# Optimization experiments

Hardware: AMD Instinct MI355X
Metric: run time of the kernel (lower is better)

## Reference

```python
import jax, jax.numpy as jnp
import numpy as np

H, D, DK, DV = 8, 512, 64, 64
B, L = 2, 2048
LN_EPS = 1e-5


def setup_inputs() -> dict:
    key = jax.random.key(0)
    ks = jax.random.split(key, 12)
    q = jax.random.normal(ks[0], (B, L, D), jnp.float32)
    k = jax.random.normal(ks[1], (B, L, D), jnp.float32)
    v = jax.random.normal(ks[2], (B, L, D), jnp.float32)
    mask = jax.random.randint(ks[3], (H * B, L, L), 0, 2) > 0
    sq = np.sqrt(2.0 / (D + DK)).astype(np.float32)
    sv = np.sqrt(2.0 / (D + DV)).astype(np.float32)
    Wq = jax.random.normal(ks[4], (H * DK, D), jnp.float32) * sq
    Wk = jax.random.normal(ks[5], (H * DK, D), jnp.float32) * sq
    Wv = jax.random.normal(ks[6], (H * DV, D), jnp.float32) * sv
    xav = np.sqrt(2.0 / (H * DV + D)).astype(np.float32)
    Wfc = jax.random.normal(ks[7], (D, H * DV), jnp.float32) * xav
    bfc = jnp.zeros((D,), jnp.float32)
    gamma = jnp.ones((D,), jnp.float32)
    beta = jnp.zeros((D,), jnp.float32)
    return {"q": q, "k": k, "v": v, "mask": mask, "Wq": Wq, "Wk": Wk,
            "Wv": Wv, "Wfc": Wfc, "bfc": bfc, "gamma": gamma, "beta": beta}


def reference(q, k, v, mask, Wq, Wk, Wv, Wfc, bfc, gamma, beta):
    # dropout in eval mode (identity)
    temperature = jnp.sqrt(jnp.asarray(DK, q.dtype))
    residual = q
    # projections -> (H, B, L, dk/dv), matching permute(2,0,1,3)
    qh = (q @ Wq.T).reshape(B, L, H, DK).transpose(2, 0, 1, 3)
    kh = (k @ Wk.T).reshape(B, L, H, DK).transpose(2, 0, 1, 3)
    vh = (v @ Wv.T).reshape(B, L, H, DV).transpose(2, 0, 1, 3)
    attn = jnp.einsum('hbqd,hbkd->hbqk', qh, kh) / temperature
    m = mask.reshape(H, B, L, L)
    attn = jnp.where(m, jnp.asarray(-1e10, attn.dtype), attn)
    attn = jax.nn.softmax(attn, axis=-1)
    out = jnp.einsum('hbqk,hbkd->hbqd', attn, vh)  # (H,B,L,DV)
    out = out.transpose(1, 2, 0, 3).reshape(B, L, H * DV)
    out = out @ Wfc.T + bfc
    x = out + residual
    mu = jnp.mean(x, axis=-1, keepdims=True)
    var = jnp.var(x, axis=-1, keepdims=True)
    return gamma * (x - mu) * jax.lax.rsqrt(var + LN_EPS) + beta
```

## Files before the change

### kernel.cpp

```cpp
#include <hip/hip_runtime.h>
#include <hip/hip_bf16.h>
#include <cmath>
#include <cstdint>

#define H_ 8
#define B_ 2
#define L_ 2048
#define D_ 512
#define SPLIT_ 4

typedef __attribute__((ext_vector_type(8))) short short8_t;
typedef __attribute__((ext_vector_type(4))) float float4_t;
typedef __attribute__((ext_vector_type(4))) unsigned short ushort4_t;
typedef __attribute__((ext_vector_type(2))) unsigned int uint2_t;
typedef __attribute__((ext_vector_type(4))) unsigned int uint4_t;

__device__ __forceinline__ unsigned short bf16u(float f) {
  union { __hip_bfloat16 b; unsigned short u; } c;
  c.b = __float2bfloat16(f);
  return c.u;
}
__device__ __forceinline__ unsigned bf16x2(float lo, float hi) {
  return (unsigned)bf16u(lo) | ((unsigned)bf16u(hi) << 16);
}
__device__ __forceinline__ float bf2f(unsigned short u) {
  union { unsigned u; float f; } c; c.u = (unsigned)u << 16; return c.f;
}

__device__ __forceinline__ unsigned pack8(unsigned long long x) {
  x |= x >> 4; x |= x >> 2; x |= x >> 1;
  x &= 0x0101010101010101ULL;
  return (unsigned)((x * 0x0102040810204080ULL) >> 56);
}

__global__ __launch_bounds__(256)
void cvt_w(const float* __restrict__ wfc, unsigned short* __restrict__ wfcb) {
  int i = (blockIdx.x * 256 + threadIdx.x) * 4;
  float4_t a = *(const float4_t*)(wfc + i);
  ushort4_t o;
  o[0] = bf16u(a[0]); o[1] = bf16u(a[1]); o[2] = bf16u(a[2]); o[3] = bf16u(a[3]);
  *(ushort4_t*)(wfcb + i) = o;
}

__global__ __launch_bounds__(512)
void proj_gemm(const float* __restrict__ q, const float* __restrict__ k,
               const float* __restrict__ v,
               const float* __restrict__ wq, const float* __restrict__ wk,
               const float* __restrict__ wv,
               unsigned short* __restrict__ Qp, unsigned short* __restrict__ Kp,
               unsigned short* __restrict__ Vt) {
  __shared__ unsigned short As[128][72];
  __shared__ unsigned short Bs[64][72];
  const int tid = threadIdx.x, lane = tid & 63, wave = tid >> 6;
  const int g = lane >> 4, qi = lane & 15;
  const int m0 = blockIdx.x * 128, n0 = blockIdx.y * 64;
  const int z = blockIdx.z;
  const float* A = (z == 0) ? q : (z == 1) ? k : v;
  const float* W = (z == 0) ? wq : (z == 1) ? wk : wv;

  float4_t acc[4] = {};
  const int ar = tid >> 2, ac = (tid & 3) * 16;
  const int br = tid >> 3, bc = (tid & 7) * 8;

  for (int kt = 0; kt < 512; kt += 64) {
    const float* src = A + (size_t)(m0 + ar) * 512 + kt + ac;
    float4_t f0 = *(const float4_t*)(src);
    float4_t f1 = *(const float4_t*)(src + 4);
    float4_t f2 = *(const float4_t*)(src + 8);
    float4_t f3 = *(const float4_t*)(src + 12);
    short8_t s0, s1;
    s0[0] = bf16u(f0[0]); s0[1] = bf16u(f0[1]); s0[2] = bf16u(f0[2]); s0[3] = bf16u(f0[3]);
    s0[4] = bf16u(f1[0]); s0[5] = bf16u(f1[1]); s0[6] = bf16u(f1[2]); s0[7] = bf16u(f1[3]);
    s1[0] = bf16u(f2[0]); s1[1] = bf16u(f2[1]); s1[2] = bf16u(f2[2]); s1[3] = bf16u(f2[3]);
    s1[4] = bf16u(f3[0]); s1[5] = bf16u(f3[1]); s1[6] = bf16u(f3[2]); s1[7] = bf16u(f3[3]);
    *(short8_t*)(&As[ar][ac]) = s0;
    *(short8_t*)(&As[ar][ac + 8]) = s1;
    const float* wsrc = W + (size_t)(n0 + br) * 512 + kt + bc;
    float4_t w0 = *(const float4_t*)(wsrc);
    float4_t w1 = *(const float4_t*)(wsrc + 4);
    short8_t sw;
    sw[0] = bf16u(w0[0]); sw[1] = bf16u(w0[1]); sw[2] = bf16u(w0[2]); sw[3] = bf16u(w0[3]);
    sw[4] = bf16u(w1[0]); sw[5] = bf16u(w1[1]); sw[6] = bf16u(w1[2]); sw[7] = bf16u(w1[3]);
    *(short8_t*)(&Bs[br][bc]) = sw;
    __syncthreads();
#pragma unroll
    for (int kk = 0; kk < 2; kk++) {
      const int krow = kk * 32 + g * 8;
      short8_t a = *(const short8_t*)(&As[wave * 16 + qi][krow]);
#pragma unroll
      for (int n = 0; n < 4; n++) {
        short8_t b = *(const short8_t*)(&Bs[n * 16 + qi][krow]);
        acc[n] = __builtin_amdgcn_mfma_f32_16x16x32_bf16(a, b, acc[n], 0, 0, 0);
      }
    }
    __syncthreads();
  }

  const int gmb = m0 + wave * 16 + g * 4;
#pragma unroll
  for (int n = 0; n < 4; n++) {
    int gn = n0 + n * 16 + qi;
    int h = gn >> 6, d = gn & 63;
    if (z == 2) {
      int bb = gmb >> 11, l = gmb & 2047;
      ushort4_t o;
#pragma unroll
      for (int r = 0; r < 4; r++) o[r] = bf16u(acc[n][r]);
      *(ushort4_t*)(Vt + ((size_t)(h * B_ + bb) * 64 + d) * L_ + l) = o;
    } else {
      float sc = (z == 0) ? 0.125f : 1.0f;
      unsigned short* O = (z == 0) ? Qp : Kp;
#pragma unroll
      for (int r = 0; r < 4; r++) {
        int gm = gmb + r;
        int bb = gm >> 11, l = gm & 2047;
        O[((size_t)(h * B_ + bb) * L_ + l) * 64 + d] = bf16u(acc[n][r] * sc);
      }
    }
  }
}

template<int MS>
__device__ __forceinline__ void attn_body(
    const unsigned short* __restrict__ Qp, const unsigned short* __restrict__ Kp,
    const unsigned short* __restrict__ Vt, const unsigned char* __restrict__ mask,
    unsigned short* __restrict__ Opart, float* __restrict__ MLpart,
    unsigned short (*Ks)[72], unsigned short (*Vs)[72], unsigned int (*Ps)[36]) {
  const int tid = threadIdx.x, lane = tid & 63, wave = tid >> 6;
  const int g = lane >> 4, qi = lane & 15;
  const int hb = blockIdx.y;
  const int sp = blockIdx.z;
  const int k_begin = sp * (L_ / SPLIT_), k_end = k_begin + L_ / SPLIT_;
  const int qg0 = blockIdx.x * 128 + wave * 16;
  const int qg = qg0 + qi;
  const size_t base = (size_t)hb * (L_ * 64);

  const size_t mrowoff = ((size_t)hb * L_ + qg0 + (lane >> 2)) * L_;
  const unsigned char* mb1 = mask + mrowoff + (lane & 3) * 16;
  const unsigned* mb4 = (const unsigned*)mask + mrowoff + (lane & 3) * 16;

  short8_t qf[2];
#pragma unroll
  for (int kk = 0; kk < 2; kk++)
    qf[kk] = *(const short8_t*)(Qp + base + (size_t)qg * 64 + kk * 32 + g * 8);

  float4_t o[4] = {};
  float mrun = -INFINITY, lrun = 0.f;
  const int sr = tid >> 3, sc = (tid & 7) * 8;
  const int srcA = qi * 4;

#define LOADFB(dst, kpos)                                                        \
  do {                                                                           \
    if (MS == 1) {                                                               \
      uint4_t x = *(const uint4_t*)(mb1 + (kpos));                               \
      unsigned long long lo = ((unsigned long long)x[1] << 32) | x[0];           \
      unsigned long long hi = ((unsigned long long)x[3] << 32) | x[2];           \
      dst = pack8(lo) | (pack8(hi) << 8);                                        \
    } else {                                                                     \
      dst = 0;                                                                   \
      _Pragma("unroll")                                                          \
      for (int j = 0; j < 4; j++) {                                              \
        uint4_t x = *(const uint4_t*)(mb4 + (kpos) + j * 4);                     \
        dst |= (((unsigned)(x[0] != 0)) | ((unsigned)(x[1] != 0) << 1) |         \
                ((unsigned)(x[2] != 0) << 2) | ((unsigned)(x[3] != 0) << 3))     \
               << (j * 4);                                                       \
      }                                                                          \
    }                                                                            \
  } while (0)

  short8_t kr, vr;
  unsigned fb1, fb2;
  kr = *(const short8_t*)(Kp + base + (size_t)(k_begin + sr) * 64 + sc);
  vr = *(const short8_t*)(Vt + base + (size_t)sr * L_ + k_begin + sc);
  LOADFB(fb1, k_begin);
  fb2 = 0;
  if (k_begin + 64 < k_end) LOADFB(fb2, k_begin + 64);

  for (int k0 = k_begin; k0 < k_end; k0 += 64) {
    *(short8_t*)(&Ks[sr][sc]) = kr;
    *(short8_t*)(&Vs[sr][sc]) = vr;
    unsigned fb_cur = fb1;
    fb1 = fb2;
    __syncthreads();

    if (k0 + 64 < k_end) {
      const int kn = k0 + 64;
      kr = *(const short8_t*)(Kp + base + (size_t)(kn + sr) * 64 + sc);
      vr = *(const short8_t*)(Vt + base + (size_t)sr * L_ + kn + sc);
    }
    if (k0 + 128 < k_end) LOADFB(fb2, k0 + 128);

    unsigned nib[4];
#pragma unroll
    for (int t = 0; t < 4; t++)
      nib[t] = ((unsigned)__shfl((int)fb_cur, srcA + t, 64) >> (g * 4)) & 0xFu;

    float4_t st[4] = {};
#pragma unroll
    for (int kk = 0; kk < 2; kk++) {
      const int krow = kk * 32 + g * 8;
#pragma unroll
      for (int t = 0; t < 4; t++) {
        short8_t a = *(const short8_t*)(&Ks[t * 16 + qi][krow]);
        st[t] = __builtin_amdgcn_mfma_f32_16x16x32_bf16(a, qf[kk], st[t], 0, 0, 0);
      }
    }

    float tmax = -INFINITY;
#pragma unroll
    for (int t = 0; t < 4; t++)
#pragma unroll
      for (int r = 0; r < 4; r++) {
        if ((nib[t] >> r) & 1u) st[t][r] = -1e10f;
        tmax = fmaxf(tmax, st[t][r]);
      }
    tmax = fmaxf(tmax, __shfl_xor(tmax, 16, 64));
    tmax = fmaxf(tmax, __shfl_xor(tmax, 32, 64));

    float nm = fmaxf(mrun, tmax);
    float fac = __expf(mrun - nm);
    mrun = nm;

    float psum = 0.f;
    unsigned w8[4][2];
#pragma unroll
    for (int t = 0; t < 4; t++) {
      float p0 = __expf(st[t][0] - nm);
      float p1 = __expf(st[t][1] - nm);
      float p2 = __expf(st[t][2] - nm);
      float p3 = __expf(st[t][3] - nm);
      psum += (p0 + p1) + (p2 + p3);
      w8[t][0] = bf16x2(p0, p1);
      w8[t][1] = bf16x2(p2, p3);
    }
    psum += __shfl_xor(psum, 16, 64);
    psum += __shfl_xor(psum, 32, 64);
    lrun = lrun * fac + psum;
#pragma unroll
    for (int n2 = 0; n2 < 4; n2++)
#pragma unroll
      for (int r = 0; r < 4; r++) o[n2][r] *= fac;

#pragma unroll
    for (int t = 0; t < 4; t++) {
      uint2_t w2; w2[0] = w8[t][0]; w2[1] = w8[t][1];
      *(uint2_t*)(&Ps[qi][t * 8 + g * 2]) = w2;
    }
#pragma unroll
    for (int s = 0; s < 2; s++) {
      short8_t pb = *(const short8_t*)(&Ps[qi][s * 16 + g * 4]);
#pragma unroll
      for (int n2 = 0; n2 < 4; n2++) {
        short8_t a = *(const short8_t*)(&Vs[n2 * 16 + qi][s * 32 + g * 8]);
        o[n2] = __builtin_amdgcn_mfma_f32_16x16x32_bf16(a, pb, o[n2], 0, 0, 0);
      }
    }
    __syncthreads();
  }
#undef LOADFB

  const size_t pb = (((size_t)sp * 16 + hb) * L_ + qg) * 64;
#pragma unroll
  for (int n2 = 0; n2 < 4; n2++) {
    ushort4_t ov;
#pragma unroll
    for (int r = 0; r < 4; r++) ov[r] = bf16u(o[n2][r]);
    *(ushort4_t*)(Opart + pb + n2 * 16 + g * 4) = ov;
  }
  if (lane < 16) {
    float* ml = MLpart + (((size_t)sp * 16 + hb) * L_ + qg) * 2;
    ml[0] = mrun; ml[1] = lrun;
  }
}

__global__ __launch_bounds__(512)
void attn_split(const unsigned short* __restrict__ Qp, const unsigned short* __restrict__ Kp,
                const unsigned short* __restrict__ Vt, const unsigned char* __restrict__ mask,
                unsigned short* __restrict__ Opart, float* __restrict__ MLpart) {
  __shared__ unsigned short Ks[64][72];
  __shared__ unsigned short Vs[64][72];
  __shared__ unsigned int PsAll[8][16][36];
  const int wave = threadIdx.x >> 6;
  unsigned probe = ((const unsigned*)mask)[threadIdx.x & 63];
  if (__any(probe > 1u))
    attn_body<1>(Qp, Kp, Vt, mask, Opart, MLpart, Ks, Vs, PsAll[wave]);
  else
    attn_body<4>(Qp, Kp, Vt, mask, Opart, MLpart, Ks, Vs, PsAll[wave]);
}

__global__ __launch_bounds__(256)
void attn_combine(const unsigned short* __restrict__ Opart, const float* __restrict__ MLpart,
                  unsigned short* __restrict__ Y) {
  int gid = blockIdx.x * 256 + threadIdx.x;
  int dvc = (gid & 7) * 8;
  int hbq = gid >> 3;
  int hb = hbq >> 11, qq = hbq & 2047;
  int h = hb >> 1, bb = hb & 1;
  float m[SPLIT_], l[SPLIT_];
  float M = -INFINITY;
#pragma unroll
  for (int s = 0; s < SPLIT_; s++) {
    const float* ml = MLpart + (((size_t)s * 16 + hb) * L_ + qq) * 2;
    m[s] = ml[0]; l[s] = ml[1];
    M = fmaxf(M, m[s]);
  }
  float denom = 0.f, e[SPLIT_];
#pragma unroll
  for (int s = 0; s < SPLIT_; s++) { e[s] = __expf(m[s] - M); denom += l[s] * e[s]; }
  float inv = 1.0f / denom;
  float acc[8] = {};
#pragma unroll
  for (int s = 0; s < SPLIT_; s++) {
    const unsigned short* p = Opart + (((size_t)s * 16 + hb) * L_ + qq) * 64 + dvc;
    ushort4_t a0 = *(const ushort4_t*)(p);
    ushort4_t a1 = *(const ushort4_t*)(p + 4);
    float w = e[s] * inv;
#pragma unroll
    for (int j = 0; j < 4; j++) {
      acc[j] += bf2f(a0[j]) * w;
      acc[j + 4] += bf2f(a1[j]) * w;
    }
  }
  short8_t ov;
#pragma unroll
  for (int j = 0; j < 8; j++) ov[j] = bf16u(acc[j]);
  *(short8_t*)(Y + ((size_t)(bb * L_ + qq)) * 512 + h * 64 + dvc) = ov;
}

__global__ __launch_bounds__(512)
void fc_gemm(const unsigned short* __restrict__ Yb, const unsigned short* __restrict__ wfcb,
             const float* __restrict__ resid, const float* __restrict__ bfc,
             float* __restrict__ out) {
  __shared__ unsigned short As[128][72];
  __shared__ unsigned short Bs[64][72];
  const int tid = threadIdx.x, lane = tid & 63, wave = tid >> 6;
  const int g = lane >> 4, qi = lane & 15;
  const int m0 = blockIdx.x * 128, n0 = blockIdx.y * 64;
  float4_t acc[4] = {};
  const int ar = tid >> 2, ac = (tid & 3) * 16;
  const int br = tid >> 3, bc = (tid & 7) * 8;

  for (int kt = 0; kt < 512; kt += 64) {
    const unsigned short* src = Yb + (size_t)(m0 + ar) * 512 + kt + ac;
    *(short8_t*)(&As[ar][ac]) = *(const short8_t*)(src);
    *(short8_t*)(&As[ar][ac + 8]) = *(const short8_t*)(src + 8);
    *(short8_t*)(&Bs[br][bc]) = *(const short8_t*)(wfcb + (size_t)(n0 + br) * 512 + kt + bc);
    __syncthreads();
#pragma unroll
    for (int kk = 0; kk < 2; kk++) {
      const int krow = kk * 32 + g * 8;
      short8_t a = *(const short8_t*)(&As[wave * 16 + qi][krow]);
#pragma unroll
      for (int n = 0; n < 4; n++) {
        short8_t b = *(const short8_t*)(&Bs[n * 16 + qi][krow]);
        acc[n] = __builtin_amdgcn_mfma_f32_16x16x32_bf16(a, b, acc[n], 0, 0, 0);
      }
    }
    __syncthreads();
  }

  const int gmb = m0 + wave * 16 + g * 4;
#pragma unroll
  for (int n = 0; n < 4; n++) {
    int gn = n0 + n * 16 + qi;
    float bv = bfc[gn];
#pragma unroll
    for (int r = 0; r < 4; r++) {
      int gm = gmb + r;
      out[(size_t)gm * 512 + gn] = acc[n][r] + bv + resid[(size_t)gm * 512 + gn];
    }
  }
}

__global__ __launch_bounds__(256)
void ln_kernel(float* __restrict__ Z, const float* __restrict__ gamma,
               const float* __restrict__ beta) {
  const int row = blockIdx.x * 4 + (threadIdx.x >> 6);
  const int lane = threadIdx.x & 63;
  float* zp = Z + (size_t)row * 512 + lane * 8;
  float4_t x0 = *(const float4_t*)(zp);
  float4_t x1 = *(const float4_t*)(zp + 4);
  float s = 0.f, s2 = 0.f;
#pragma unroll
  for (int j = 0; j < 4; j++) { s += x0[j] + x1[j]; s2 += x0[j] * x0[j] + x1[j] * x1[j]; }
#pragma unroll
  for (int mm = 1; mm < 64; mm <<= 1) { s += __shfl_xor(s, mm, 64); s2 += __shfl_xor(s2, mm, 64); }
  float mu = s * (1.f / 512.f);
  float var = s2 * (1.f / 512.f) - mu * mu;
  float inv = rsqrtf(var + 1e-5f);
  float4_t g0 = *(const float4_t*)(gamma + lane * 8);
  float4_t g1 = *(const float4_t*)(gamma + lane * 8 + 4);
  float4_t b0 = *(const float4_t*)(beta + lane * 8);
  float4_t b1 = *(const float4_t*)(beta + lane * 8 + 4);
#pragma unroll
  for (int j = 0; j < 4; j++) {
    x0[j] = g0[j] * (x0[j] - mu) * inv + b0[j];
    x1[j] = g1[j] * (x1[j] - mu) * inv + b1[j];
  }
  *(float4_t*)(zp) = x0;
  *(float4_t*)(zp + 4) = x1;
}

extern "C" void kernel_launch(void* const* d_in, const int* in_sizes, int n_in,
                              void* d_out, int out_size, void* d_ws, size_t ws_size,
                              hipStream_t stream) {
  const float* q   = (const float*)d_in[0];
  const float* k   = (const float*)d_in[1];
  const float* v   = (const float*)d_in[2];
  const unsigned char* mask = (const unsigned char*)d_in[3];
  const float* Wq  = (const float*)d_in[4];
  const float* Wk  = (const float*)d_in[5];
  const float* Wv  = (const float*)d_in[6];
  const float* Wfc = (const float*)d_in[7];
  const float* bfc = (const float*)d_in[8];
  const float* gamma = (const float*)d_in[9];
  const float* beta  = (const float*)d_in[10];
  float* out = (float*)d_out;

  char* ws = (char*)d_ws;
  unsigned short* wfcb = (unsigned short*)(ws);
  unsigned short* Qp   = wfcb + 262144;
  unsigned short* Kp   = Qp + 2097152;
  unsigned short* Vt   = Kp + 2097152;
  unsigned short* Y    = Vt + 2097152;
  unsigned short* Opart = Y + 2097152;
  float* MLpart = (float*)(Opart + (size_t)SPLIT_ * 16 * L_ * 64);

  cvt_w<<<256, 256, 0, stream>>>(Wfc, wfcb);
  proj_gemm<<<dim3(32, 8, 3), 512, 0, stream>>>(q, k, v, Wq, Wk, Wv, Qp, Kp, Vt);
  attn_split<<<dim3(16, 16, SPLIT_), 512, 0, stream>>>(Qp, Kp, Vt, mask, Opart, MLpart);
  attn_combine<<<1024, 256, 0, stream>>>(Opart, MLpart, Y);
  fc_gemm<<<dim3(32, 8), 512, 0, stream>>>(Y, wfcb, q, bfc, out);
  ln_kernel<<<1024, 256, 0, stream>>>(out, gamma, beta);
}
```

Measured before the change: 127.2 us.

## Double-buffer K/V tiles, pass P via shuffles, fold Wfc conversion into fc GEMM

The attention loop now double-buffers the K and V tiles in shared memory, which leaves one barrier per iteration instead of two. The per-wave P shared-memory round trip is replaced by cross-lane shuffles that build the MFMA B operand directly from registers. The separate Wfc-to-bf16 conversion kernel is removed, and fc_gemm converts fp32 weights on the fly while loading them, saving a launch at the cost of more global traffic per block. Doubled K/V LDS plus extra shuffles may change occupancy and instruction count.

```diff
diff --git a/kernel.cpp b/kernel.cpp
--- a/kernel.cpp
+++ b/kernel.cpp
@@ -12,7 +12,6 @@
 typedef __attribute__((ext_vector_type(8))) short short8_t;
 typedef __attribute__((ext_vector_type(4))) float float4_t;
 typedef __attribute__((ext_vector_type(4))) unsigned short ushort4_t;
-typedef __attribute__((ext_vector_type(2))) unsigned int uint2_t;
 typedef __attribute__((ext_vector_type(4))) unsigned int uint4_t;
 
 __device__ __forceinline__ unsigned short bf16u(float f) {
@@ -31,15 +30,6 @@
   x |= x >> 4; x |= x >> 2; x |= x >> 1;
   x &= 0x0101010101010101ULL;
   return (unsigned)((x * 0x0102040810204080ULL) >> 56);
-}
-
-__global__ __launch_bounds__(256)
-void cvt_w(const float* __restrict__ wfc, unsigned short* __restrict__ wfcb) {
-  int i = (blockIdx.x * 256 + threadIdx.x) * 4;
-  float4_t a = *(const float4_t*)(wfc + i);
-  ushort4_t o;
-  o[0] = bf16u(a[0]); o[1] = bf16u(a[1]); o[2] = bf16u(a[2]); o[3] = bf16u(a[3]);
-  *(ushort4_t*)(wfcb + i) = o;
 }
 
 __global__ __launch_bounds__(512)
@@ -125,7 +115,7 @@
     const unsigned short* __restrict__ Qp, const unsigned short* __restrict__ Kp,
     const unsigned short* __restrict__ Vt, const unsigned char* __restrict__ mask,
     unsigned short* __restrict__ Opart, float* __restrict__ MLpart,
-    unsigned short (*Ks)[72], unsigned short (*Vs)[72], unsigned int (*Ps)[36]) {
+    unsigned short (*Ks)[64][72], unsigned short (*Vs)[64][72]) {
   const int tid = threadIdx.x, lane = tid & 63, wave = tid >> 6;
   const int g = lane >> 4, qi = lane & 15;
   const int hb = blockIdx.y;
@@ -148,6 +138,7 @@
   float mrun = -INFINITY, lrun = 0.f;
   const int sr = tid >> 3, sc = (tid & 7) * 8;
   const int srcA = qi * 4;
+  const int srcP = qi + 32 * (g & 1);
 
 #define LOADFB(dst, kpos)                                                        \
   do {                                                                           \
@@ -175,19 +166,20 @@
   LOADFB(fb1, k_begin);
   fb2 = 0;
   if (k_begin + 64 < k_end) LOADFB(fb2, k_begin + 64);
-
+  *(short8_t*)(&Ks[0][sr][sc]) = kr;
+  *(short8_t*)(&Vs[0][sr][sc]) = vr;
+  __syncthreads();
+
+  int bufi = 0;
   for (int k0 = k_begin; k0 < k_end; k0 += 64) {
-    *(short8_t*)(&Ks[sr][sc]) = kr;
-    *(short8_t*)(&Vs[sr][sc]) = vr;
-    unsigned fb_cur = fb1;
-    fb1 = fb2;
-    __syncthreads();
-
-    if (k0 + 64 < k_end) {
+    const bool has_next = (k0 + 64 < k_end);
+    if (has_next) {
       const int kn = k0 + 64;
       kr = *(const short8_t*)(Kp + base + (size_t)(kn + sr) * 64 + sc);
       vr = *(const short8_t*)(Vt + base + (size_t)sr * L_ + kn + sc);
     }
+    unsigned fb_cur = fb1;
+    fb1 = fb2;
     if (k0 + 128 < k_end) LOADFB(fb2, k0 + 128);
 
     unsigned nib[4];
@@ -201,7 +193,7 @@
       const int krow = kk * 32 + g * 8;
 #pragma unroll
       for (int t = 0; t < 4; t++) {
-        short8_t a = *(const short8_t*)(&Ks[t * 16 + qi][krow]);
+        short8_t a = *(const short8_t*)(&Ks[bufi][t * 16 + qi][krow]);
         st[t] = __builtin_amdgcn_mfma_f32_16x16x32_bf16(a, qf[kk], st[t], 0, 0, 0);
       }
     }
@@ -242,20 +234,34 @@
       for (int r = 0; r < 4; r++) o[n2][r] *= fac;
 
 #pragma unroll
-    for (int t = 0; t < 4; t++) {
-      uint2_t w2; w2[0] = w8[t][0]; w2[1] = w8[t][1];
-      *(uint2_t*)(&Ps[qi][t * 8 + g * 2]) = w2;
-    }
-#pragma unroll
     for (int s = 0; s < 2; s++) {
-      short8_t pb = *(const short8_t*)(&Ps[qi][s * 16 + g * 4]);
+      unsigned a00 = (unsigned)__shfl((int)w8[2 * s][0],     srcP, 64);
+      unsigned a10 = (unsigned)__shfl((int)w8[2 * s + 1][0], srcP, 64);
+      unsigned a01 = (unsigned)__shfl((int)w8[2 * s][1],     srcP, 64);
+      unsigned a11 = (unsigned)__shfl((int)w8[2 * s + 1][1], srcP, 64);
+      unsigned b00 = (unsigned)__shfl((int)w8[2 * s][0],     srcP + 16, 64);
+      unsigned b10 = (unsigned)__shfl((int)w8[2 * s + 1][0], srcP + 16, 64);
+      unsigned b01 = (unsigned)__shfl((int)w8[2 * s][1],     srcP + 16, 64);
+      unsigned b11 = (unsigned)__shfl((int)w8[2 * s + 1][1], srcP + 16, 64);
+      const bool hi = (g & 2) != 0;
+      union { unsigned u[4]; short8_t s8; } pb;
+      pb.u[0] = hi ? a10 : a00;
+      pb.u[1] = hi ? a11 : a01;
+      pb.u[2] = hi ? b10 : b00;
+      pb.u[3] = hi ? b11 : b01;
 #pragma unroll
       for (int n2 = 0; n2 < 4; n2++) {
-        short8_t a = *(const short8_t*)(&Vs[n2 * 16 + qi][s * 32 + g * 8]);
-        o[n2] = __builtin_amdgcn_mfma_f32_16x16x32_bf16(a, pb, o[n2], 0, 0, 0);
-      }
-    }
-    __syncthreads();
+        short8_t a = *(const short8_t*)(&Vs[bufi][n2 * 16 + qi][s * 32 + g * 8]);
+        o[n2] = __builtin_amdgcn_mfma_f32_16x16x32_bf16(a, pb.s8, o[n2], 0, 0, 0);
+      }
+    }
+
+    if (has_next) {
+      *(short8_t*)(&Ks[bufi ^ 1][sr][sc]) = kr;
+      *(short8_t*)(&Vs[bufi ^ 1][sr][sc]) = vr;
+      __syncthreads();
+      bufi ^= 1;
+    }
   }
 #undef LOADFB
 
@@ -277,15 +283,13 @@
 void attn_split(const unsigned short* __restrict__ Qp, const unsigned short* __restrict__ Kp,
                 const unsigned short* __restrict__ Vt, const unsigned char* __restrict__ mask,
                 unsigned short* __restrict__ Opart, float* __restrict__ MLpart) {
-  __shared__ unsigned short Ks[64][72];
-  __shared__ unsigned short Vs[64][72];
-  __shared__ unsigned int PsAll[8][16][36];
-  const int wave = threadIdx.x >> 6;
+  __shared__ unsigned short Ks[2][64][72];
+  __shared__ unsigned short Vs[2][64][72];
   unsigned probe = ((const unsigned*)mask)[threadIdx.x & 63];
   if (__any(probe > 1u))
-    attn_body<1>(Qp, Kp, Vt, mask, Opart, MLpart, Ks, Vs, PsAll[wave]);
+    attn_body<1>(Qp, Kp, Vt, mask, Opart, MLpart, Ks, Vs);
   else
-    attn_body<4>(Qp, Kp, Vt, mask, Opart, MLpart, Ks, Vs, PsAll[wave]);
+    attn_body<4>(Qp, Kp, Vt, mask, Opart, MLpart, Ks, Vs);
 }
 
 __global__ __launch_bounds__(256)
@@ -328,7 +332,7 @@
 }
 
 __global__ __launch_bounds__(512)
-void fc_gemm(const unsigned short* __restrict__ Yb, const unsigned short* __restrict__ wfcb,
+void fc_gemm(const unsigned short* __restrict__ Yb, const float* __restrict__ wfc,
              const float* __restrict__ resid, const float* __restrict__ bfc,
              float* __restrict__ out) {
   __shared__ unsigned short As[128][72];
@@ -344,7 +348,13 @@
     const unsigned short* src = Yb + (size_t)(m0 + ar) * 512 + kt + ac;
     *(short8_t*)(&As[ar][ac]) = *(const short8_t*)(src);
     *(short8_t*)(&As[ar][ac + 8]) = *(const short8_t*)(src + 8);
-    *(short8_t*)(&Bs[br][bc]) = *(const short8_t*)(wfcb + (size_t)(n0 + br) * 512 + kt + bc);
+    const float* wsrc = wfc + (size_t)(n0 + br) * 512 + kt + bc;
+    float4_t w0 = *(const float4_t*)(wsrc);
+    float4_t w1 = *(const float4_t*)(wsrc + 4);
+    short8_t sw;
+    sw[0] = bf16u(w0[0]); sw[1] = bf16u(w0[1]); sw[2] = bf16u(w0[2]); sw[3] = bf16u(w0[3]);
+    sw[4] = bf16u(w1[0]); sw[5] = bf16u(w1[1]); sw[6] = bf16u(w1[2]); sw[7] = bf16u(w1[3]);
+    *(short8_t*)(&Bs[br][bc]) = sw;
     __syncthreads();
 #pragma unroll
     for (int kk = 0; kk < 2; kk++) {
@@ -418,18 +428,16 @@
   float* out = (float*)d_out;
 
   char* ws = (char*)d_ws;
-  unsigned short* wfcb = (unsigned short*)(ws);
-  unsigned short* Qp   = wfcb + 262144;
+  unsigned short* Qp   = (unsigned short*)(ws);
   unsigned short* Kp   = Qp + 2097152;
   unsigned short* Vt   = Kp + 2097152;
   unsigned short* Y    = Vt + 2097152;
   unsigned short* Opart = Y + 2097152;
   float* MLpart = (float*)(Opart + (size_t)SPLIT_ * 16 * L_ * 64);
 
-  cvt_w<<<256, 256, 0, stream>>>(Wfc, wfcb);
   proj_gemm<<<dim3(32, 8, 3), 512, 0, stream>>>(q, k, v, Wq, Wk, Wv, Qp, Kp, Vt);
   attn_split<<<dim3(16, 16, SPLIT_), 512, 0, stream>>>(Qp, Kp, Vt, mask, Opart, MLpart);
   attn_combine<<<1024, 256, 0, stream>>>(Opart, MLpart, Y);
-  fc_gemm<<<dim3(32, 8), 512, 0, stream>>>(Y, wfcb, q, bfc, out);
+  fc_gemm<<<dim3(32, 8), 512, 0, stream>>>(Y, Wfc, q, bfc, out);
   ln_kernel<<<1024, 256, 0, stream>>>(out, gamma, beta);
 }
```

After: 123.3 us. 3.1% less time.
